# Performance work log

Hardware: AMD Instinct MI355X
Metric: run time of the kernel (lower is better)

Reference implementation:

```python
import jax, jax.numpy as jnp
import numpy as np

D, H, K = 384, 6, 8
B, NQ, NK = 4, 2048, 2048
EPS = 1e-5


def _ln(x, s, b):
    m = jnp.mean(x, axis=-1, keepdims=True)
    v = jnp.mean((x - m) ** 2, axis=-1, keepdims=True)
    return (x - m) * jax.lax.rsqrt(v + EPS) * s + b


def _mha(q, k, v, Wo, bo):
    # q,k,v: [B, N, D]
    dh = D // H
    qh = q.reshape(q.shape[0], q.shape[1], H, dh).transpose(0, 2, 1, 3)
    kh = k.reshape(k.shape[0], k.shape[1], H, dh).transpose(0, 2, 1, 3)
    vh = v.reshape(v.shape[0], v.shape[1], H, dh).transpose(0, 2, 1, 3)
    scores = jnp.einsum('bhqd,bhkd->bhqk', qh, kh) / jnp.sqrt(jnp.asarray(dh, q.dtype))
    attn = jax.nn.softmax(scores, axis=-1)
    out = jnp.einsum('bhqk,bhkd->bhqd', attn, vh)
    out = out.transpose(0, 2, 1, 3).reshape(q.shape[0], q.shape[1], D)
    return out @ Wo + bo


def _knn_edge(q_coords, k_coords, q_feats, k_feats):
    # coords: [B, N, 3]; feats: [B, N, D]. EdgeConv-style feature:
    # concat(neighbor_feat - center_feat, center_feat) -> [B, Nq, K, 2D]
    d2 = (jnp.sum(q_coords ** 2, -1)[:, :, None]
          + jnp.sum(k_coords ** 2, -1)[:, None, :]
          - 2.0 * jnp.einsum('bqc,bkc->bqk', q_coords, k_coords))
    _, idx = jax.lax.top_k(-d2, K)  # [B, Nq, K] nearest neighbors in key set
    neigh = jax.vmap(lambda f, i: f[i])(k_feats, idx)  # [B, Nq, K, D]
    center = jnp.broadcast_to(q_feats[:, :, None, :], neigh.shape)
    return jnp.concatenate([neigh - center, center], axis=-1)


def setup_inputs() -> dict:
    key = jax.random.key(0)
    ks = jax.random.split(key, 24)
    s = 0.02
    return {
        'query_points': jax.random.normal(ks[0], (B, 3 + D, NQ), jnp.float32),
        'key_points': jax.random.normal(ks[1], (B, 3 + D, NK), jnp.float32),
        'ln_in_s': jnp.ones((D,), jnp.float32), 'ln_in_b': jnp.zeros((D,), jnp.float32),
        'qkv_W': jax.random.normal(ks[2], (D, 3 * D), jnp.float32) * s,
        'attn_out_W': jax.random.normal(ks[3], (D, D), jnp.float32) * s,
        'attn_out_b': jnp.zeros((D,), jnp.float32),
        'ff_W1': jax.random.normal(ks[4], (D, 2 * D), jnp.float32) * s,
        'ff_b1': jnp.zeros((2 * D,), jnp.float32),
        'ff_W2': jax.random.normal(ks[5], (2 * D, D), jnp.float32) * s,
        'ff_b2': jnp.zeros((D,), jnp.float32),
        'ffn_s': jnp.ones((D,), jnp.float32), 'ffn_b': jnp.zeros((D,), jnp.float32),
        'knn1_W': jax.random.normal(ks[6], (2 * D, D), jnp.float32) * s,
        'knn1_b': jnp.zeros((D,), jnp.float32),
        'knn2_W': jax.random.normal(ks[7], (2 * D, D), jnp.float32) * s,
        'knn2_b': jnp.zeros((D,), jnp.float32),
        'self_merge_W': jax.random.normal(ks[8], (2 * D, D), jnp.float32) * s,
        'self_merge_b': jnp.zeros((D,), jnp.float32),
        'cross_merge_W': jax.random.normal(ks[9], (2 * D, D), jnp.float32) * s,
        'cross_merge_b': jnp.zeros((D,), jnp.float32),
        'cnq_s': jnp.ones((D,), jnp.float32), 'cnq_b': jnp.zeros((D,), jnp.float32),
        'cnk_s': jnp.ones((D,), jnp.float32), 'cnk_b': jnp.zeros((D,), jnp.float32),
        'cq_W': jax.random.normal(ks[10], (D, D), jnp.float32) * s,
        'ck_W': jax.random.normal(ks[11], (D, D), jnp.float32) * s,
        'cv_W': jax.random.normal(ks[12], (D, D), jnp.float32) * s,
    }


def reference(query_points, key_points, ln_in_s, ln_in_b, qkv_W, attn_out_W,
              attn_out_b, ff_W1, ff_b1, ff_W2, ff_b2, ffn_s, ffn_b,
              knn1_W, knn1_b, knn2_W, knn2_b, self_merge_W, self_merge_b,
              cross_merge_W, cross_merge_b, cnq_s, cnq_b, cnk_s, cnk_b,
              cq_W, ck_W, cv_W):
    qp = jnp.transpose(query_points, (0, 2, 1))  # [B, Nq, 3+D]
    kp = jnp.transpose(key_points, (0, 2, 1))    # [B, Nk, 3+D]
    q_coords, q_feats = qp[..., :3], qp[..., 3:]
    k_coords, k_feats = kp[..., :3], kp[..., 3:]

    # --- self attention + self kNN geometry ---
    norm_f = _ln(q_feats, ln_in_s, ln_in_b)
    qkv = norm_f @ qkv_W
    q, k, v = jnp.split(qkv, 3, axis=-1)
    attn_f = _mha(q, k, v, attn_out_W, attn_out_b)

    edge = _knn_edge(q_coords, q_coords, norm_f, norm_f)          # [B,Nq,K,2D]
    geom = jax.nn.leaky_relu(edge @ knn1_W + knn1_b, 0.2)
    geom = jnp.max(geom, axis=2)                                   # [B,Nq,D]

    attn_f = jnp.concatenate([attn_f, geom], axis=-1) @ self_merge_W + self_merge_b
    q_feats = attn_f + q_feats

    # --- cross attention + cross kNN geometry ---
    nq = _ln(q_feats, cnq_s, cnq_b)
    nk = _ln(k_feats, cnk_s, cnk_b)
    cross_f = _mha(nq @ cq_W, nk @ ck_W, nk @ cv_W, attn_out_W, attn_out_b)

    cedge = _knn_edge(q_coords, k_coords, nq, nk)                  # [B,Nq,K,2D]
    cgeom = jax.nn.leaky_relu(cedge @ knn2_W + knn2_b, 0.2)
    cgeom = jnp.max(cgeom, axis=2)

    cross_f = jnp.concatenate([cross_f, cgeom], axis=-1) @ cross_merge_W + cross_merge_b
    q_feats = q_feats + cross_f

    # --- feed forward ---
    h = _ln(q_feats, ffn_s, ffn_b)
    q_feats = q_feats + (jax.nn.gelu(h @ ff_W1 + ff_b1) @ ff_W2 + ff_b2)

    out = jnp.concatenate([q_coords, q_feats], axis=-1)
    return jnp.transpose(out, (0, 2, 1))  # [B, 3+D, Nq]
```

## Files before the change

### kernel.cpp

```cpp
#include <hip/hip_runtime.h>
#include <cstdint>
#include <cstddef>

#define NB 4
#define NN 2048
#define DD 384
#define NH 6

typedef float f4 __attribute__((ext_vector_type(4)));
typedef float f32x4 __attribute__((ext_vector_type(4)));
typedef short bf16x8 __attribute__((ext_vector_type(8)));
typedef unsigned u32x2 __attribute__((ext_vector_type(2)));

__device__ __forceinline__ float gelu_t(float x) {
  float x3 = x*x*x;
  return 0.5f*x*(1.0f + tanhf(0.7978845608028654f*(x + 0.044715f*x3)));
}

__device__ __forceinline__ unsigned short f2b(float f) {
  unsigned u = __builtin_bit_cast(unsigned, f);
  u += 0x7fffu + ((u >> 16) & 1u);
  return (unsigned short)(u >> 16);
}

__device__ __forceinline__ float b2f(unsigned short u) {
  return __builtin_bit_cast(float, ((unsigned)u) << 16);
}

__device__ __forceinline__ unsigned cvtpk(float a, float b) {
  unsigned r;
  asm("v_cvt_pk_bf16_f32 %0, %1, %2" : "=v"(r) : "v"(a), "v"(b));
  return r;
}

typedef __attribute__((address_space(1))) const void gvoid_t;
typedef __attribute__((address_space(3))) void lvoid_t;
__device__ __forceinline__ void gl16(const void* g, void* l) {
  __builtin_amdgcn_global_load_lds((gvoid_t*)g, (lvoid_t*)l, 16, 0, 0);
}

__device__ __forceinline__ unsigned long long shfl_xor_u64(unsigned long long v, int m) {
  unsigned lo = (unsigned)v, hi = (unsigned)(v >> 32);
  lo = (unsigned)__shfl_xor((int)lo, m);
  hi = (unsigned)__shfl_xor((int)hi, m);
  return ((unsigned long long)hi << 32) | lo;
}

__global__ __launch_bounds__(256) void split_k(const float* __restrict__ pts,
                                               float* __restrict__ coords,
                                               float* __restrict__ feats) {
  __shared__ float t[32][33];
  int b = blockIdx.z;
  int c0 = blockIdx.x*32, n0 = blockIdx.y*32;
  int tx = threadIdx.x, ty = threadIdx.y;
#pragma unroll
  for (int i = 0; i < 4; ++i) {
    int c = c0 + ty + i*8;
    if (c < 387) t[ty+i*8][tx] = pts[((size_t)b*387 + c)*NN + n0 + tx];
  }
  __syncthreads();
#pragma unroll
  for (int i = 0; i < 4; ++i) {
    int n = n0 + ty + i*8;
    int c = c0 + tx;
    if (c < 387) {
      float v = t[tx][ty+i*8];
      if (c < 3) coords[((size_t)b*NN + n)*4 + c] = v;
      else       feats[((size_t)b*NN + n)*DD + (c-3)] = v;
    }
    if (c0 == 0 && tx == 3) {
      float x = t[0][ty+i*8], y = t[1][ty+i*8], z = t[2][ty+i*8];
      coords[((size_t)b*NN + n)*4 + 3] = x*x + y*y + z*z;
    }
  }
}

__global__ __launch_bounds__(256) void pack_k(const float* __restrict__ coords,
                                              const float* __restrict__ feats,
                                              float* __restrict__ out) {
  __shared__ float t[32][33];
  int b = blockIdx.z;
  int c0 = blockIdx.x*32, n0 = blockIdx.y*32;
  int tx = threadIdx.x, ty = threadIdx.y;
#pragma unroll
  for (int i = 0; i < 4; ++i) {
    int n = n0 + ty + i*8;
    int c = c0 + tx;
    if (c < 387) {
      float v = (c < 3) ? coords[((size_t)b*NN + n)*4 + c]
                        : feats[((size_t)b*NN + n)*DD + (c-3)];
      t[tx][ty+i*8] = v;
    }
  }
  __syncthreads();
#pragma unroll
  for (int i = 0; i < 4; ++i) {
    int c = c0 + ty + i*8;
    if (c < 387) out[((size_t)b*387 + c)*NN + n0 + tx] = t[ty+i*8][tx];
  }
}

__device__ __forceinline__ void ln_body(const float* __restrict__ x,
                                        const float* __restrict__ g,
                                        const float* __restrict__ bb,
                                        unsigned short* __restrict__ o,
                                        int row) {
  int lane = threadIdx.x & 63;
  const float* xr = x + (size_t)row*DD;
  float v[6]; float s = 0.f;
#pragma unroll
  for (int i = 0; i < 6; ++i) { v[i] = xr[lane + i*64]; s += v[i]; }
#pragma unroll
  for (int off = 1; off < 64; off <<= 1) s += __shfl_xor(s, off);
  float mean = s * (1.f/384.f);
  float s2 = 0.f;
#pragma unroll
  for (int i = 0; i < 6; ++i) { float d = v[i] - mean; s2 += d*d; }
#pragma unroll
  for (int off = 1; off < 64; off <<= 1) s2 += __shfl_xor(s2, off);
  float rs = rsqrtf(s2*(1.f/384.f) + 1e-5f);
  unsigned short* orow = o + (size_t)row*DD;
#pragma unroll
  for (int i = 0; i < 6; ++i) {
    int c = lane + i*64;
    orow[c] = f2b((v[i]-mean)*rs*g[c] + bb[c]);
  }
}

__global__ __launch_bounds__(256) void ln_k(const float* __restrict__ x,
                                            const float* __restrict__ g,
                                            const float* __restrict__ bb,
                                            unsigned short* __restrict__ o) {
  ln_body(x, g, bb, o, blockIdx.x*4 + (threadIdx.x >> 6));
}

__global__ __launch_bounds__(256) void ln2_k(const float* __restrict__ x1,
                                             const float* __restrict__ g1,
                                             const float* __restrict__ b1,
                                             unsigned short* __restrict__ o1,
                                             const float* __restrict__ x2,
                                             const float* __restrict__ g2,
                                             const float* __restrict__ b2,
                                             unsigned short* __restrict__ o2) {
  int row = blockIdx.x*4 + (threadIdx.x >> 6);
  if (blockIdx.y == 0) ln_body(x1, g1, b1, o1, row);
  else                 ln_body(x2, g2, b2, o2, row);
}

struct WSrcs { const float* p[13]; };

__global__ __launch_bounds__(256) void wtrans_k(WSrcs srcs, unsigned short* __restrict__ dst) {
  constexpr int KK[13]  = {384,384,384,384,768,384,384,384,384,384,768,384,768};
  constexpr int NW[13]  = {1152,384,384,384,384,384,384,384,384,384,384,768,384};
  constexpr int MD[13]  = {0,0,2,0,0,0,0,0,0,2,0,0,0};
  constexpr int OFF[13] = {0,442368,589824,737280,884736,1179648,1327104,1474560,
                           1622016,1769472,1916928,2211840,2506752};
  constexpr int PFX[14] = {0,432,576,720,864,1152,1296,1440,1584,1728,1872,2160,2448,2736};
  int bid = blockIdx.x;
  int e = 0;
  while (bid >= PFX[e+1]) ++e;
  int t = bid - PFX[e];
  int K = KK[e], N = NW[e];
  int ntiles = N >> 5;
  int kt = t / ntiles, nt = t - kt*ntiles;
  const float* src = srcs.p[e];
  __shared__ float T[32][33];
  int tx = threadIdx.x & 31, ty = threadIdx.x >> 5;
  int n = nt*32 + tx;
#pragma unroll
  for (int i = 0; i < 4; ++i) {
    int k = kt*32 + ty + i*8;
    float v = src[(size_t)k*N + n];
    if (MD[e] == 2) v = src[(size_t)(k+384)*N + n] - v;
    T[ty+i*8][tx] = v;
  }
  __syncthreads();
#pragma unroll
  for (int i = 0; i < 4; ++i) {
    int nn = nt*32 + ty + i*8;
    int kk = kt*32 + tx;
    dst[(size_t)OFF[e] + (size_t)nn*K + kk] = f2b(T[tx][ty+i*8]);
  }
}

template<int ACT, int ACC, int OB, int HALFM>
__global__ __launch_bounds__(256) void mgemm_k(const unsigned short* __restrict__ A, int lda,
                                               const unsigned short* __restrict__ Wt,
                                               const float* __restrict__ bias,
                                               void* __restrict__ Cv, int ldc, int cofs,
                                               int Kd) {
  constexpr int BM   = HALFM ? 64 : 128;
  constexpr int MT   = HALFM ? 2 : 4;
  constexpr int AG   = HALFM ? 2 : 4;
  constexpr int ABUF = BM*128;
  constexpr int BUFSZ = ABUF + 8192;
  __shared__ char lds[2*BUFSZ];
  int tid = threadIdx.x;
  int lane = tid & 63, w = tid >> 6, g = lane >> 4, c = lane & 15;
  int wr = w >> 1, wc = w & 1;
  int m0 = blockIdx.y*BM, n0 = blockIdx.x*64;
  int lrow = lane >> 3;
  int cswz = ((lane & 7) ^ lrow)*8;

  f32x4 acc[MT][2];
#pragma unroll
  for (int mt = 0; mt < MT; ++mt)
#pragma unroll
    for (int nt = 0; nt < 2; ++nt) acc[mt][nt] = 0.f;

  int KT = Kd >> 6;
  {
    char* As = lds; char* Bs = lds + ABUF;
#pragma unroll
    for (int i = 0; i < AG; ++i) {
      int rb = i*32 + w*8;
      gl16(A + (size_t)(m0 + rb + lrow)*lda + cswz, As + rb*128);
    }
#pragma unroll
    for (int i = 0; i < 2; ++i) {
      int rb = i*32 + w*8;
      gl16(Wt + (size_t)(n0 + rb + lrow)*Kd + cswz, Bs + rb*128);
    }
  }
  __syncthreads();

  for (int kt = 0; kt < KT; ++kt) {
    char* Asc = lds + (kt & 1)*BUFSZ;
    char* Bsc = Asc + ABUF;
    if (kt + 1 < KT) {
      char* Asn = lds + ((kt + 1) & 1)*BUFSZ;
      char* Bsn = Asn + ABUF;
      int k0 = (kt + 1)*64;
#pragma unroll
      for (int i = 0; i < AG; ++i) {
        int rb = i*32 + w*8;
        gl16(A + (size_t)(m0 + rb + lrow)*lda + k0 + cswz, Asn + rb*128);
      }
#pragma unroll
      for (int i = 0; i < 2; ++i) {
        int rb = i*32 + w*8;
        gl16(Wt + (size_t)(n0 + rb + lrow)*Kd + k0 + cswz, Bsn + rb*128);
      }
    }
#pragma unroll
    for (int kb = 0; kb < 2; ++kb) {
      bf16x8 af[MT], bfr[2];
#pragma unroll
      for (int mt = 0; mt < MT; ++mt) {
        int row = wr*(BM/2) + mt*16 + c;
        int ch = (kb*4 + g) ^ (row & 7);
        af[mt] = *(const bf16x8*)(Asc + row*128 + ch*16);
      }
#pragma unroll
      for (int nt = 0; nt < 2; ++nt) {
        int row = wc*32 + nt*16 + c;
        int ch = (kb*4 + g) ^ (row & 7);
        bfr[nt] = *(const bf16x8*)(Bsc + row*128 + ch*16);
      }
#pragma unroll
      for (int mt = 0; mt < MT; ++mt)
#pragma unroll
        for (int nt = 0; nt < 2; ++nt)
          acc[mt][nt] = __builtin_amdgcn_mfma_f32_16x16x32_bf16(af[mt], bfr[nt], acc[mt][nt], 0, 0, 0);
    }
    __syncthreads();
  }

#pragma unroll
  for (int mt = 0; mt < MT; ++mt) {
#pragma unroll
    for (int nt = 0; nt < 2; ++nt) {
      int coln = n0 + wc*32 + nt*16 + c;
      float bval = bias ? bias[coln] : 0.f;
#pragma unroll
      for (int r = 0; r < 4; ++r) {
        int m = m0 + wr*(BM/2) + mt*16 + 4*g + r;
        float t = acc[mt][nt][r] + bval;
        if (ACT == 1) t = gelu_t(t);
        if (OB) {
          ((unsigned short*)Cv)[(size_t)m*ldc + cofs + coln] = f2b(t);
        } else {
          float* cp = (float*)Cv + (size_t)m*ldc + cofs + coln;
          if (ACC) t += *cp;
          *cp = t;
        }
      }
    }
  }
}

struct FSegs {
  const unsigned short* A[5];
  unsigned short* out[5];
  int ldc[5];
  int cofs[5];
};

__global__ __launch_bounds__(256) void fgemm_k(FSegs fs, const unsigned short* __restrict__ Wt) {
  __shared__ char lds[49152];
  int tid = threadIdx.x;
  int lane = tid & 63, w = tid >> 6, g = lane >> 4, c = lane & 15;
  int wr = w >> 1, wc = w & 1;
  int m0 = blockIdx.y*128, n0 = blockIdx.x*64;
  int seg = n0 / 384;
  const unsigned short* A = fs.A[seg];
  int lrow = lane >> 3;
  int cswz = ((lane & 7) ^ lrow)*8;

  f32x4 acc[4][2];
#pragma unroll
  for (int mt = 0; mt < 4; ++mt)
#pragma unroll
    for (int nt = 0; nt < 2; ++nt) acc[mt][nt] = 0.f;

  {
    char* As = lds; char* Bs = lds + 16384;
#pragma unroll
    for (int i = 0; i < 4; ++i) {
      int rb = i*32 + w*8;
      gl16(A + (size_t)(m0 + rb + lrow)*384 + cswz, As + rb*128);
    }
#pragma unroll
    for (int i = 0; i < 2; ++i) {
      int rb = i*32 + w*8;
      gl16(Wt + (size_t)(n0 + rb + lrow)*384 + cswz, Bs + rb*128);
    }
  }
  __syncthreads();

  for (int kt = 0; kt < 6; ++kt) {
    char* Asc = lds + (kt & 1)*24576;
    char* Bsc = Asc + 16384;
    if (kt + 1 < 6) {
      char* Asn = lds + ((kt + 1) & 1)*24576;
      char* Bsn = Asn + 16384;
      int k0 = (kt + 1)*64;
#pragma unroll
      for (int i = 0; i < 4; ++i) {
        int rb = i*32 + w*8;
        gl16(A + (size_t)(m0 + rb + lrow)*384 + k0 + cswz, Asn + rb*128);
      }
#pragma unroll
      for (int i = 0; i < 2; ++i) {
        int rb = i*32 + w*8;
        gl16(Wt + (size_t)(n0 + rb + lrow)*384 + k0 + cswz, Bsn + rb*128);
      }
    }
#pragma unroll
    for (int kb = 0; kb < 2; ++kb) {
      bf16x8 af[4], bfr[2];
#pragma unroll
      for (int mt = 0; mt < 4; ++mt) {
        int row = wr*64 + mt*16 + c;
        int ch = (kb*4 + g) ^ (row & 7);
        af[mt] = *(const bf16x8*)(Asc + row*128 + ch*16);
      }
#pragma unroll
      for (int nt = 0; nt < 2; ++nt) {
        int row = wc*32 + nt*16 + c;
        int ch = (kb*4 + g) ^ (row & 7);
        bfr[nt] = *(const bf16x8*)(Bsc + row*128 + ch*16);
      }
#pragma unroll
      for (int mt = 0; mt < 4; ++mt)
#pragma unroll
        for (int nt = 0; nt < 2; ++nt)
          acc[mt][nt] = __builtin_amdgcn_mfma_f32_16x16x32_bf16(af[mt], bfr[nt], acc[mt][nt], 0, 0, 0);
    }
    __syncthreads();
  }

  if (seg == 2) {
    unsigned short* vtp = fs.out[2];
    int bb = m0 >> 11;
    int tokb = (m0 & 2047) + wr*64 + 4*g;
#pragma unroll
    for (int mt = 0; mt < 4; ++mt) {
#pragma unroll
      for (int nt = 0; nt < 2; ++nt) {
        int cseg = (n0 - 768) + wc*32 + nt*16 + c;
        int h = cseg >> 6, d = cseg & 63;
        u32x2 pv;
        pv[0] = cvtpk(acc[mt][nt][0], acc[mt][nt][1]);
        pv[1] = cvtpk(acc[mt][nt][2], acc[mt][nt][3]);
        *(u32x2*)(vtp + ((size_t)((bb*NH + h)*64 + d))*NN + tokb + mt*16) = pv;
      }
    }
    return;
  }

  unsigned short* outp = fs.out[seg];
  int ldcs = fs.ldc[seg];
  int cbase = fs.cofs[seg] + (n0 - seg*384);
#pragma unroll
  for (int mt = 0; mt < 4; ++mt) {
#pragma unroll
    for (int nt = 0; nt < 2; ++nt) {
      int coln = cbase + wc*32 + nt*16 + c;
#pragma unroll
      for (int r = 0; r < 4; ++r) {
        int m = m0 + wr*64 + mt*16 + 4*g + r;
        outp[(size_t)m*ldcs + coln] = f2b(acc[mt][nt][r]);
      }
    }
  }
}

__global__ __launch_bounds__(256) void flashm_k(const unsigned short* __restrict__ qkvb,
                                                const unsigned short* __restrict__ vt,
                                                unsigned short* __restrict__ o) {
  __shared__ char smem[40960];
  char* PT = smem + 32768;
  int bid = blockIdx.x;
  int s = (bid & 7)*96 + (bid >> 3);
  int qt = s & 31; int hb = s >> 5;
  int h = hb % NH, b = hb / NH;
  int q0 = qt*64;
  int tid = threadIdx.x;
  int w = tid >> 6, lane = tid & 63, g = lane >> 4, c = lane & 15;
  int lrow = lane >> 3;
  int gsw = ((lane & 7) ^ lrow)*8;

  const unsigned short* kbase = qkvb + (size_t)b*NN*1152 + 384 + h*64;
  const unsigned short* vbase = vt + ((size_t)(b*NH + h))*64*NN;

  bf16x8 qf[2];
  {
    const unsigned short* qrow = qkvb + ((size_t)(b*NN + q0 + w*16 + c))*1152 + h*64;
    qf[0] = *(const bf16x8*)(qrow + 8*g);
    qf[1] = *(const bf16x8*)(qrow + 32 + 8*g);
  }
  f32x4 oacc[4];
#pragma unroll
  for (int i = 0; i < 4; ++i) oacc[i] = 0.f;
  float lsum = 0.f;

#define FSTAGE(bf, ktb) { \
    char* KB = smem + (bf)*16384; char* VB = KB + 8192; \
    gl16(kbase + (size_t)((ktb) + w*16 + lrow)*1152 + gsw,     KB + (w*16)*128); \
    gl16(kbase + (size_t)((ktb) + w*16 + 8 + lrow)*1152 + gsw, KB + (w*16+8)*128); \
    gl16(vbase + (size_t)(w*16 + lrow)*NN + (ktb) + gsw,       VB + (w*16)*128); \
    gl16(vbase + (size_t)(w*16 + 8 + lrow)*NN + (ktb) + gsw,   VB + (w*16+8)*128); }

  FSTAGE(0, 0);
  __syncthreads();

  for (int kt = 0; kt < 32; ++kt) {
    if (kt + 1 < 32) FSTAGE((kt + 1) & 1, (kt + 1)*64);
    char* KTc = smem + (kt & 1)*16384;
    char* VTc = KTc + 8192;

    f32x4 sT[4];
#pragma unroll
    for (int nt = 0; nt < 4; ++nt) sT[nt] = 0.f;
#pragma unroll
    for (int nt = 0; nt < 4; ++nt) {
      int krow = nt*16 + c;
#pragma unroll
      for (int kb = 0; kb < 2; ++kb) {
        int ch = ((kb*4 + g) ^ (krow & 7))*16;
        bf16x8 kf_ = *(const bf16x8*)(KTc + krow*128 + ch);
        sT[nt] = __builtin_amdgcn_mfma_f32_16x16x32_bf16(kf_, qf[kb], sT[nt], 0, 0, 0);
      }
    }

    int prow = w*16 + c;
    int pswz = (c & 7) << 4;
#pragma unroll
    for (int nt = 0; nt < 4; ++nt) {
      float p0 = __builtin_amdgcn_exp2f(sT[nt][0] * 0.18033688011112042f);
      float p1 = __builtin_amdgcn_exp2f(sT[nt][1] * 0.18033688011112042f);
      float p2 = __builtin_amdgcn_exp2f(sT[nt][2] * 0.18033688011112042f);
      float p3 = __builtin_amdgcn_exp2f(sT[nt][3] * 0.18033688011112042f);
      lsum += (p0 + p1) + (p2 + p3);
      u32x2 pk;
      pk[0] = cvtpk(p0, p1);
      pk[1] = cvtpk(p2, p3);
      *(u32x2*)(PT + prow*128 + ((nt*32 + 8*g) ^ pswz)) = pk;
    }

    bf16x8 pb[2];
#pragma unroll
    for (int kb = 0; kb < 2; ++kb)
      pb[kb] = *(const bf16x8*)(PT + prow*128 + (((kb*4 + g) ^ (c & 7))*16));

#pragma unroll
    for (int dt = 0; dt < 4; ++dt) {
      int vrow = dt*16 + c;
#pragma unroll
      for (int kb = 0; kb < 2; ++kb) {
        int ch = ((kb*4 + g) ^ (vrow & 7))*16;
        bf16x8 vf = *(const bf16x8*)(VTc + vrow*128 + ch);
        oacc[dt] = __builtin_amdgcn_mfma_f32_16x16x32_bf16(vf, pb[kb], oacc[dt], 0, 0, 0);
      }
    }
    __syncthreads();
  }
#undef FSTAGE

  lsum += __shfl_xor(lsum, 16);
  lsum += __shfl_xor(lsum, 32);
  float inv = 1.f / lsum;
  size_t orow = ((size_t)b*NN + q0 + w*16 + c)*DD + h*64;
#pragma unroll
  for (int dt = 0; dt < 4; ++dt) {
    u32x2 ov;
    ov[0] = cvtpk(oacc[dt][0]*inv, oacc[dt][1]*inv);
    ov[1] = cvtpk(oacc[dt][2]*inv, oacc[dt][3]*inv);
    *(u32x2*)(o + orow + dt*16 + 4*g) = ov;
  }
}

__global__ __launch_bounds__(256) void knn2_k(const float* __restrict__ qc4,
                                              const float* __restrict__ kc4,
                                              int* __restrict__ idx1,
                                              int* __restrict__ idx2) {
  __shared__ unsigned long long sbuf[4][64];
  const float* kcs = blockIdx.y ? kc4 : qc4;
  int* idxo = blockIdx.y ? idx2 : idx1;
  int lane = threadIdx.x & 63;
  int w = threadIdx.x >> 6;
  int q = blockIdx.x*4 + w;
  int b = q >> 11;
  f4 qv = *(const f4*)(qc4 + (size_t)q*4);
  float mx_ = -2.f*qv[0], my_ = -2.f*qv[1], mz_ = -2.f*qv[2];
  const float* kb = kcs + (size_t)b*NN*4;

  float fv[32];
  float fm = INFINITY;
#pragma unroll
  for (int i = 0; i < 32; ++i) {
    f4 kv = *(const f4*)(kb + (size_t)(lane + i*64)*4);
    float f = fmaf(mx_, kv[0], fmaf(my_, kv[1], fmaf(mz_, kv[2], kv[3])));
    fv[i] = f;
    fm = fminf(fm, f);
  }

  {
    float v = fm;
#pragma unroll
    for (int k = 2; k <= 64; k <<= 1) {
#pragma unroll
      for (int j = k >> 1; j >= 1; j >>= 1) {
        float p = __shfl_xor(v, j);
        bool tmin = (((lane & k) == 0) == ((lane & j) == 0));
        v = tmin ? fminf(v, p) : fmaxf(v, p);
      }
    }
    fm = __shfl(v, 7);
  }
  float T = fm;

  int cnt = 0;
#pragma unroll
  for (int i = 0; i < 32; ++i) {
    bool p = fv[i] <= T;
    unsigned long long mask = __ballot(p);
    if (mask) {
      if (p) {
        int off = cnt + (int)__popcll(mask & ((1ull << lane) - 1ull));
        unsigned u = __builtin_bit_cast(unsigned, fv[i]);
        u ^= 0x80000000u | (unsigned)((int)u >> 31);
        if (off < 64)
          sbuf[w][off] = ((unsigned long long)u << 32) | (unsigned)(lane + i*64);
      }
      cnt += (int)__popcll(mask);
    }
  }

  unsigned long long key = ~0ull;
  if (lane < cnt && lane < 64) key = sbuf[w][lane];
#pragma unroll
  for (int k = 2; k <= 64; k <<= 1) {
#pragma unroll
    for (int j = k >> 1; j >= 1; j >>= 1) {
      unsigned long long p = shfl_xor_u64(key, j);
      bool tmin = (((lane & k) == 0) == ((lane & j) == 0));
      bool less = key < p;
      unsigned long long mn = less ? key : p;
      unsigned long long mx = less ? p : key;
      key = tmin ? mn : mx;
    }
  }
  if (lane < 8) idxo[(size_t)q*8 + lane] = (int)(unsigned)key;
}

__global__ __launch_bounds__(384) void geom_k(const unsigned short* __restrict__ GCb,
                                              const float* __restrict__ bias,
                                              const int* __restrict__ idx,
                                              unsigned short* __restrict__ out) {
  int q = blockIdx.x;
  int b = q >> 11;
  int d = threadIdx.x;
  float c = b2f(GCb[(size_t)q*768 + 384 + d]) + bias[d];
  float mx = -INFINITY;
#pragma unroll
  for (int kn = 0; kn < 8; ++kn) {
    int j = idx[(size_t)q*8 + kn];
    float gg = b2f(GCb[((size_t)(b << 11) + j)*768 + d]);
    float y = gg + c;
    y = (y > 0.f) ? y : 0.2f*y;
    mx = fmaxf(mx, y);
  }
  out[(size_t)q*768 + 384 + d] = f2b(mx);
}

extern "C" void kernel_launch(void* const* d_in, const int* in_sizes, int n_in,
                              void* d_out, int out_size, void* d_ws, size_t ws_size,
                              hipStream_t stream) {
  (void)in_sizes; (void)n_in; (void)out_size; (void)ws_size;
  const float* qpts  = (const float*)d_in[0];
  const float* kpts  = (const float*)d_in[1];
  const float* ln_s  = (const float*)d_in[2];
  const float* ln_b  = (const float*)d_in[3];
  const float* qkvW  = (const float*)d_in[4];
  const float* Wo    = (const float*)d_in[5];
  const float* bo    = (const float*)d_in[6];
  const float* ffW1  = (const float*)d_in[7];
  const float* ffb1  = (const float*)d_in[8];
  const float* ffW2  = (const float*)d_in[9];
  const float* ffb2  = (const float*)d_in[10];
  const float* ffns  = (const float*)d_in[11];
  const float* ffnb  = (const float*)d_in[12];
  const float* knn1W = (const float*)d_in[13];
  const float* knn1b = (const float*)d_in[14];
  const float* knn2W = (const float*)d_in[15];
  const float* knn2b = (const float*)d_in[16];
  const float* smW   = (const float*)d_in[17];
  const float* smb   = (const float*)d_in[18];
  const float* cmW   = (const float*)d_in[19];
  const float* cmb   = (const float*)d_in[20];
  const float* cnqs  = (const float*)d_in[21];
  const float* cnqb  = (const float*)d_in[22];
  const float* cnks  = (const float*)d_in[23];
  const float* cnkb  = (const float*)d_in[24];
  const float* cqW   = (const float*)d_in[25];
  const float* ckW   = (const float*)d_in[26];
  const float* cvW   = (const float*)d_in[27];

  float* ws = (float*)d_ws;
  float* qc4  = ws;
  float* kc4  = qc4 + 32768;
  float* qf   = kc4 + 32768;
  float* kf   = qf + 3145728;
  unsigned short* nrmb = (unsigned short*)(kf + 3145728);
  unsigned short* nkb  = (unsigned short*)(kf + 3145728 + 1572864);
  float* qkv = kf + 3145728 + 1572864 + 1572864;
  unsigned short* qkvb   = (unsigned short*)qkv;
  unsigned short* attnGb = (unsigned short*)qkv;
  unsigned short* vtb    = (unsigned short*)(qkv + 4718592);
  unsigned short* wtb    = (unsigned short*)(qkv + 4718592 + 1572864);
  unsigned short* attnOb = (unsigned short*)(qkv + 4718592 + 1572864 + 1400832);
  unsigned short* GCbb   = (unsigned short*)((float*)attnOb + 1572864);
  int* idx1 = (int*)((float*)GCbb + 3145728);
  int* idx2 = idx1 + 65536;

  const int W_FA=0, W_WO=737280, W_SM=884736, W_FB=1179648,
            W_CM=1916928, W_FF1=2211840, W_FF2=2506752;

  WSrcs srcs;
  srcs.p[0]=qkvW; srcs.p[1]=knn1W; srcs.p[2]=knn1W; srcs.p[3]=Wo; srcs.p[4]=smW;
  srcs.p[5]=cqW; srcs.p[6]=ckW; srcs.p[7]=cvW; srcs.p[8]=knn2W; srcs.p[9]=knn2W;
  srcs.p[10]=cmW; srcs.p[11]=ffW1; srcs.p[12]=ffW2;
  wtrans_k<<<2736, 256, 0, stream>>>(srcs, wtb);

  dim3 tgrid(13, 64, NB), tblk(32, 8);
  split_k<<<tgrid, tblk, 0, stream>>>(qpts, qc4, qf);
  split_k<<<tgrid, tblk, 0, stream>>>(kpts, kc4, kf);

  knn2_k<<<dim3(2048, 2), 256, 0, stream>>>(qc4, kc4, idx1, idx2);

  dim3 mg384h(6, 128), mg768(12, 64), fg(30, 64);

  ln_k<<<2048, 256, 0, stream>>>(qf, ln_s, ln_b, nrmb);
  {
    FSegs fa;
    for (int s = 0; s < 5; ++s) fa.A[s] = nrmb;
    fa.out[0] = qkvb; fa.ldc[0] = 1152; fa.cofs[0] = 0;
    fa.out[1] = qkvb; fa.ldc[1] = 1152; fa.cofs[1] = 384;
    fa.out[2] = vtb;  fa.ldc[2] = 0;    fa.cofs[2] = 0;
    fa.out[3] = GCbb; fa.ldc[3] = 768;  fa.cofs[3] = 0;
    fa.out[4] = GCbb; fa.ldc[4] = 768;  fa.cofs[4] = 384;
    fgemm_k<<<fg, 256, 0, stream>>>(fa, wtb + W_FA);
  }
  flashm_k<<<768, 256, 0, stream>>>(qkvb, vtb, attnOb);
  mgemm_k<0,0,1,1><<<mg384h, 256, 0, stream>>>(attnOb, DD, wtb+W_WO, bo, attnGb, 768, 0, DD);
  geom_k<<<8192, 384, 0, stream>>>(GCbb, knn1b, idx1, attnGb);
  mgemm_k<0,1,0,1><<<mg384h, 256, 0, stream>>>(attnGb, 768, wtb+W_SM, smb, qf, DD, 0, 768);

  ln2_k<<<dim3(2048, 2), 256, 0, stream>>>(qf, cnqs, cnqb, nrmb, kf, cnks, cnkb, nkb);
  {
    FSegs fb;
    fb.A[0] = nrmb; fb.A[1] = nkb; fb.A[2] = nkb; fb.A[3] = nkb; fb.A[4] = nrmb;
    fb.out[0] = qkvb; fb.ldc[0] = 1152; fb.cofs[0] = 0;
    fb.out[1] = qkvb; fb.ldc[1] = 1152; fb.cofs[1] = 384;
    fb.out[2] = vtb;  fb.ldc[2] = 0;    fb.cofs[2] = 0;
    fb.out[3] = GCbb; fb.ldc[3] = 768;  fb.cofs[3] = 0;
    fb.out[4] = GCbb; fb.ldc[4] = 768;  fb.cofs[4] = 384;
    fgemm_k<<<fg, 256, 0, stream>>>(fb, wtb + W_FB);
  }
  flashm_k<<<768, 256, 0, stream>>>(qkvb, vtb, attnOb);
  mgemm_k<0,0,1,1><<<mg384h, 256, 0, stream>>>(attnOb, DD, wtb+W_WO, bo, attnGb, 768, 0, DD);
  geom_k<<<8192, 384, 0, stream>>>(GCbb, knn2b, idx2, attnGb);
  mgemm_k<0,1,0,1><<<mg384h, 256, 0, stream>>>(attnGb, 768, wtb+W_CM, cmb, qf, DD, 0, 768);

  ln_k<<<2048, 256, 0, stream>>>(qf, ffns, ffnb, nrmb);
  mgemm_k<1,0,1,0><<<mg768, 256, 0, stream>>>(nrmb, DD, wtb+W_FF1, ffb1, attnGb, 768, 0, DD);
  mgemm_k<0,1,0,1><<<mg384h, 256, 0, stream>>>(attnGb, 768, wtb+W_FF2, ffb2, qf, DD, 0, 768);

  pack_k<<<tgrid, tblk, 0, stream>>>(qc4, qf, (float*)d_out);
}
```

Before: 317.0 us.

## Restructure flash attention with 32x32 MFMA and split-K across wave pairs

Rewrites the attention kernel so each wave computes a 32-query by 64-key tile with 32x32x16 bf16 MFMAs. The two wave pairs each process alternate key tiles (split-K) with their own double-buffered K/V staging in 80KB of LDS. The partial outputs and row sums are merged through shared memory at the end. It also adds s_setprio around the MFMA blocks. The aim is fewer LDS reads per FLOP and more MFMA density, at the cost of more LDS (lower occupancy) and an extra reduction step.

```diff
diff --git a/kernel.cpp b/kernel.cpp
--- a/kernel.cpp
+++ b/kernel.cpp
@@ -9,6 +9,7 @@
 
 typedef float f4 __attribute__((ext_vector_type(4)));
 typedef float f32x4 __attribute__((ext_vector_type(4)));
+typedef float f32x16 __attribute__((ext_vector_type(16)));
 typedef short bf16x8 __attribute__((ext_vector_type(8)));
 typedef unsigned u32x2 __attribute__((ext_vector_type(2)));
 
@@ -409,105 +410,130 @@
 __global__ __launch_bounds__(256) void flashm_k(const unsigned short* __restrict__ qkvb,
                                                 const unsigned short* __restrict__ vt,
                                                 unsigned short* __restrict__ o) {
-  __shared__ char smem[40960];
-  char* PT = smem + 32768;
+  __shared__ char smem[81920];
   int bid = blockIdx.x;
   int s = (bid & 7)*96 + (bid >> 3);
   int qt = s & 31; int hb = s >> 5;
   int h = hb % NH, b = hb / NH;
   int q0 = qt*64;
   int tid = threadIdx.x;
-  int w = tid >> 6, lane = tid & 63, g = lane >> 4, c = lane & 15;
+  int w = tid >> 6, lane = tid & 63;
+  int p = w >> 1, sub = w & 1;
+  int col = lane & 31, hi = lane >> 5;
   int lrow = lane >> 3;
   int gsw = ((lane & 7) ^ lrow)*8;
+  int csw = (col & 7) << 4;
 
   const unsigned short* kbase = qkvb + (size_t)b*NN*1152 + 384 + h*64;
   const unsigned short* vbase = vt + ((size_t)(b*NH + h))*64*NN;
-
-  bf16x8 qf[2];
+  char* PTw = smem + 65536 + w*4096;
+
+  int qrow = q0 + sub*32 + col;
+  bf16x8 qf[4];
   {
-    const unsigned short* qrow = qkvb + ((size_t)(b*NN + q0 + w*16 + c))*1152 + h*64;
-    qf[0] = *(const bf16x8*)(qrow + 8*g);
-    qf[1] = *(const bf16x8*)(qrow + 32 + 8*g);
-  }
-  f32x4 oacc[4];
-#pragma unroll
-  for (int i = 0; i < 4; ++i) oacc[i] = 0.f;
+    const unsigned short* qr = qkvb + ((size_t)(b*NN + qrow))*1152 + h*64 + 8*hi;
+#pragma unroll
+    for (int kk = 0; kk < 4; ++kk) qf[kk] = *(const bf16x8*)(qr + 16*kk);
+  }
+  f32x16 oacc[2];
+  oacc[0] = 0.f; oacc[1] = 0.f;
   float lsum = 0.f;
 
-#define FSTAGE(bf, ktb) { \
-    char* KB = smem + (bf)*16384; char* VB = KB + 8192; \
-    gl16(kbase + (size_t)((ktb) + w*16 + lrow)*1152 + gsw,     KB + (w*16)*128); \
-    gl16(kbase + (size_t)((ktb) + w*16 + 8 + lrow)*1152 + gsw, KB + (w*16+8)*128); \
-    gl16(vbase + (size_t)(w*16 + lrow)*NN + (ktb) + gsw,       VB + (w*16)*128); \
-    gl16(vbase + (size_t)(w*16 + 8 + lrow)*NN + (ktb) + gsw,   VB + (w*16+8)*128); }
-
-  FSTAGE(0, 0);
+#define FST32(bf, t) { \
+    char* KB_ = smem + p*32768 + (bf)*16384; char* VB_ = KB_ + 8192; \
+    _Pragma("unroll") \
+    for (int i = 0; i < 4; ++i) { \
+      int rb = sub*32 + i*8; \
+      gl16(kbase + (size_t)((t)*64 + rb + lrow)*1152 + gsw, KB_ + rb*128); \
+      gl16(vbase + (size_t)(rb + lrow)*NN + (t)*64 + gsw,   VB_ + rb*128); \
+    } }
+
+  FST32(0, p);
   __syncthreads();
 
-  for (int kt = 0; kt < 32; ++kt) {
-    if (kt + 1 < 32) FSTAGE((kt + 1) & 1, (kt + 1)*64);
-    char* KTc = smem + (kt & 1)*16384;
-    char* VTc = KTc + 8192;
-
-    f32x4 sT[4];
-#pragma unroll
-    for (int nt = 0; nt < 4; ++nt) sT[nt] = 0.f;
-#pragma unroll
-    for (int nt = 0; nt < 4; ++nt) {
-      int krow = nt*16 + c;
-#pragma unroll
-      for (int kb = 0; kb < 2; ++kb) {
-        int ch = ((kb*4 + g) ^ (krow & 7))*16;
-        bf16x8 kf_ = *(const bf16x8*)(KTc + krow*128 + ch);
-        sT[nt] = __builtin_amdgcn_mfma_f32_16x16x32_bf16(kf_, qf[kb], sT[nt], 0, 0, 0);
-      }
-    }
-
-    int prow = w*16 + c;
-    int pswz = (c & 7) << 4;
-#pragma unroll
-    for (int nt = 0; nt < 4; ++nt) {
-      float p0 = __builtin_amdgcn_exp2f(sT[nt][0] * 0.18033688011112042f);
-      float p1 = __builtin_amdgcn_exp2f(sT[nt][1] * 0.18033688011112042f);
-      float p2 = __builtin_amdgcn_exp2f(sT[nt][2] * 0.18033688011112042f);
-      float p3 = __builtin_amdgcn_exp2f(sT[nt][3] * 0.18033688011112042f);
-      lsum += (p0 + p1) + (p2 + p3);
-      u32x2 pk;
-      pk[0] = cvtpk(p0, p1);
-      pk[1] = cvtpk(p2, p3);
-      *(u32x2*)(PT + prow*128 + ((nt*32 + 8*g) ^ pswz)) = pk;
-    }
-
-    bf16x8 pb[2];
-#pragma unroll
-    for (int kb = 0; kb < 2; ++kb)
-      pb[kb] = *(const bf16x8*)(PT + prow*128 + (((kb*4 + g) ^ (c & 7))*16));
-
-#pragma unroll
-    for (int dt = 0; dt < 4; ++dt) {
-      int vrow = dt*16 + c;
-#pragma unroll
-      for (int kb = 0; kb < 2; ++kb) {
-        int ch = ((kb*4 + g) ^ (vrow & 7))*16;
-        bf16x8 vf = *(const bf16x8*)(VTc + vrow*128 + ch);
-        oacc[dt] = __builtin_amdgcn_mfma_f32_16x16x32_bf16(vf, pb[kb], oacc[dt], 0, 0, 0);
-      }
-    }
+  for (int t2 = 0; t2 < 16; ++t2) {
+    if (t2 + 1 < 16) FST32((t2 + 1) & 1, 2*(t2 + 1) + p);
+    char* KB = smem + p*32768 + (t2 & 1)*16384;
+    char* VB = KB + 8192;
+
+    f32x16 sT[2];
+    sT[0] = 0.f; sT[1] = 0.f;
+    __builtin_amdgcn_s_setprio(1);
+#pragma unroll
+    for (int m = 0; m < 2; ++m) {
+#pragma unroll
+      for (int kk = 0; kk < 4; ++kk) {
+        bf16x8 kf_ = *(const bf16x8*)(KB + (32*m + col)*128 + ((32*kk + 16*hi) ^ csw));
+        sT[m] = __builtin_amdgcn_mfma_f32_32x32x16_bf16(kf_, qf[kk], sT[m], 0, 0, 0);
+      }
+    }
+    __builtin_amdgcn_s_setprio(0);
+
+#pragma unroll
+    for (int m = 0; m < 2; ++m) {
+      float pv[16];
+#pragma unroll
+      for (int r = 0; r < 16; ++r) {
+        pv[r] = __builtin_amdgcn_exp2f(sT[m][r] * 0.18033688011112042f);
+        lsum += pv[r];
+      }
+#pragma unroll
+      for (int rq = 0; rq < 4; ++rq) {
+        u32x2 pk;
+        pk[0] = cvtpk(pv[4*rq+0], pv[4*rq+1]);
+        pk[1] = cvtpk(pv[4*rq+2], pv[4*rq+3]);
+        *(u32x2*)(PTw + col*128 + ((64*m + 16*rq + 8*hi) ^ csw)) = pk;
+      }
+    }
+
+    bf16x8 pb[4];
+#pragma unroll
+    for (int kk = 0; kk < 4; ++kk)
+      pb[kk] = *(const bf16x8*)(PTw + col*128 + ((32*kk + 16*hi) ^ csw));
+
+    __builtin_amdgcn_s_setprio(1);
+#pragma unroll
+    for (int m = 0; m < 2; ++m) {
+#pragma unroll
+      for (int kk = 0; kk < 4; ++kk) {
+        bf16x8 vf = *(const bf16x8*)(VB + (32*m + col)*128 + ((32*kk + 16*hi) ^ csw));
+        oacc[m] = __builtin_amdgcn_mfma_f32_32x32x16_bf16(vf, pb[kk], oacc[m], 0, 0, 0);
+      }
+    }
+    __builtin_amdgcn_s_setprio(0);
     __syncthreads();
   }
-#undef FSTAGE
-
-  lsum += __shfl_xor(lsum, 16);
-  lsum += __shfl_xor(lsum, 32);
-  float inv = 1.f / lsum;
-  size_t orow = ((size_t)b*NN + q0 + w*16 + c)*DD + h*64;
-#pragma unroll
-  for (int dt = 0; dt < 4; ++dt) {
-    u32x2 ov;
-    ov[0] = cvtpk(oacc[dt][0]*inv, oacc[dt][1]*inv);
-    ov[1] = cvtpk(oacc[dt][2]*inv, oacc[dt][3]*inv);
-    *(u32x2*)(o + orow + dt*16 + 4*g) = ov;
+#undef FST32
+
+  if (w >= 2) {
+    float* area = (float*)(smem + (w - 2)*16384);
+#pragma unroll
+    for (int m = 0; m < 2; ++m)
+#pragma unroll
+      for (int r = 0; r < 16; ++r) area[(m*16 + r)*64 + lane] = oacc[m][r];
+    area[2048 + lane] = lsum;
+  }
+  __syncthreads();
+  if (w < 2) {
+    float* area = (float*)(smem + w*16384);
+#pragma unroll
+    for (int m = 0; m < 2; ++m)
+#pragma unroll
+      for (int r = 0; r < 16; ++r) oacc[m][r] += area[(m*16 + r)*64 + lane];
+    lsum += area[2048 + lane];
+    lsum += __shfl_xor(lsum, 32);
+    float inv = 1.f / lsum;
+    size_t orow = ((size_t)b*NN + qrow)*DD + h*64;
+#pragma unroll
+    for (int m = 0; m < 2; ++m) {
+#pragma unroll
+      for (int rq = 0; rq < 4; ++rq) {
+        u32x2 ov;
+        ov[0] = cvtpk(oacc[m][4*rq+0]*inv, oacc[m][4*rq+1]*inv);
+        ov[1] = cvtpk(oacc[m][4*rq+2]*inv, oacc[m][4*rq+3]*inv);
+        *(u32x2*)(o + orow + 32*m + 8*rq + 4*hi) = ov;
+      }
+    }
   }
 }
 
```

Measured after the change: 323.3 us. About the same (+2.0%).

## Fuse output projection with kNN geometry kernel and offload softmax row sums to MFMA

Applied to the files above, without the earlier changes.

Merges the attention output-projection GEMM and the geometry max-pool gather into one launch. GEMM tiles and geometry queries are interleaved across the grid so the two independent jobs share the GPU and one launch plus its tail is removed. The softmax scale is folded into the Q columns during the QKV GEMM epilogue, which drops a multiply per score in the flash kernel. The per-row exp sum is computed with an extra MFMA against a ones vector instead of scalar adds and cross-lane shuffles. The risks are extra rounding from scaling Q before bf16 conversion and from summing bf16-rounded probabilities, plus load imbalance in the mixed grid.

```diff
diff --git a/kernel.cpp b/kernel.cpp
--- a/kernel.cpp
+++ b/kernel.cpp
@@ -184,21 +184,20 @@
 }
 
 template<int ACT, int ACC, int OB, int HALFM>
-__global__ __launch_bounds__(256) void mgemm_k(const unsigned short* __restrict__ A, int lda,
-                                               const unsigned short* __restrict__ Wt,
-                                               const float* __restrict__ bias,
-                                               void* __restrict__ Cv, int ldc, int cofs,
-                                               int Kd) {
+__device__ __forceinline__ void mgemm_body(const unsigned short* __restrict__ A, int lda,
+                                           const unsigned short* __restrict__ Wt,
+                                           const float* __restrict__ bias,
+                                           void* __restrict__ Cv, int ldc, int cofs,
+                                           int Kd, int bx, int by, char* lds) {
   constexpr int BM   = HALFM ? 64 : 128;
   constexpr int MT   = HALFM ? 2 : 4;
   constexpr int AG   = HALFM ? 2 : 4;
   constexpr int ABUF = BM*128;
   constexpr int BUFSZ = ABUF + 8192;
-  __shared__ char lds[2*BUFSZ];
   int tid = threadIdx.x;
   int lane = tid & 63, w = tid >> 6, g = lane >> 4, c = lane & 15;
   int wr = w >> 1, wc = w & 1;
-  int m0 = blockIdx.y*BM, n0 = blockIdx.x*64;
+  int m0 = by*BM, n0 = bx*64;
   int lrow = lane >> 3;
   int cswz = ((lane & 7) ^ lrow)*8;
 
@@ -289,6 +288,18 @@
   }
 }
 
+template<int ACT, int ACC, int OB, int HALFM>
+__global__ __launch_bounds__(256) void mgemm_k(const unsigned short* __restrict__ A, int lda,
+                                               const unsigned short* __restrict__ Wt,
+                                               const float* __restrict__ bias,
+                                               void* __restrict__ Cv, int ldc, int cofs,
+                                               int Kd) {
+  constexpr int BM = HALFM ? 64 : 128;
+  __shared__ char lds[2*(BM*128 + 8192)];
+  mgemm_body<ACT,ACC,OB,HALFM>(A, lda, Wt, bias, Cv, ldc, cofs, Kd,
+                               blockIdx.x, blockIdx.y, lds);
+}
+
 struct FSegs {
   const unsigned short* A[5];
   unsigned short* out[5];
@@ -389,6 +400,7 @@
     return;
   }
 
+  float qs = (seg == 0) ? 0.18033688011112042f : 1.0f;
   unsigned short* outp = fs.out[seg];
   int ldcs = fs.ldc[seg];
   int cbase = fs.cofs[seg] + (n0 - seg*384);
@@ -400,7 +412,7 @@
 #pragma unroll
       for (int r = 0; r < 4; ++r) {
         int m = m0 + wr*64 + mt*16 + 4*g + r;
-        outp[(size_t)m*ldcs + coln] = f2b(acc[mt][nt][r]);
+        outp[(size_t)m*ldcs + coln] = f2b(acc[mt][nt][r]*qs);
       }
     }
   }
@@ -430,10 +442,14 @@
     qf[0] = *(const bf16x8*)(qrow + 8*g);
     qf[1] = *(const bf16x8*)(qrow + 32 + 8*g);
   }
+  bf16x8 onesv;
+#pragma unroll
+  for (int i = 0; i < 8; ++i) onesv[i] = (short)0x3F80;
+
   f32x4 oacc[4];
 #pragma unroll
   for (int i = 0; i < 4; ++i) oacc[i] = 0.f;
-  float lsum = 0.f;
+  f32x4 lacc = 0.f;
 
 #define FSTAGE(bf, ktb) { \
     char* KB = smem + (bf)*16384; char* VB = KB + 8192; \
@@ -468,11 +484,10 @@
     int pswz = (c & 7) << 4;
 #pragma unroll
     for (int nt = 0; nt < 4; ++nt) {
-      float p0 = __builtin_amdgcn_exp2f(sT[nt][0] * 0.18033688011112042f);
-      float p1 = __builtin_amdgcn_exp2f(sT[nt][1] * 0.18033688011112042f);
-      float p2 = __builtin_amdgcn_exp2f(sT[nt][2] * 0.18033688011112042f);
-      float p3 = __builtin_amdgcn_exp2f(sT[nt][3] * 0.18033688011112042f);
-      lsum += (p0 + p1) + (p2 + p3);
+      float p0 = __builtin_amdgcn_exp2f(sT[nt][0]);
+      float p1 = __builtin_amdgcn_exp2f(sT[nt][1]);
+      float p2 = __builtin_amdgcn_exp2f(sT[nt][2]);
+      float p3 = __builtin_amdgcn_exp2f(sT[nt][3]);
       u32x2 pk;
       pk[0] = cvtpk(p0, p1);
       pk[1] = cvtpk(p2, p3);
@@ -484,6 +499,9 @@
     for (int kb = 0; kb < 2; ++kb)
       pb[kb] = *(const bf16x8*)(PT + prow*128 + (((kb*4 + g) ^ (c & 7))*16));
 
+    lacc = __builtin_amdgcn_mfma_f32_16x16x32_bf16(onesv, pb[0], lacc, 0, 0, 0);
+    lacc = __builtin_amdgcn_mfma_f32_16x16x32_bf16(onesv, pb[1], lacc, 0, 0, 0);
+
 #pragma unroll
     for (int dt = 0; dt < 4; ++dt) {
       int vrow = dt*16 + c;
@@ -498,9 +516,7 @@
   }
 #undef FSTAGE
 
-  lsum += __shfl_xor(lsum, 16);
-  lsum += __shfl_xor(lsum, 32);
-  float inv = 1.f / lsum;
+  float inv = 1.f / lacc[0];
   size_t orow = ((size_t)b*NN + q0 + w*16 + c)*DD + h*64;
 #pragma unroll
   for (int dt = 0; dt < 4; ++dt) {
@@ -585,24 +601,63 @@
   if (lane < 8) idxo[(size_t)q*8 + lane] = (int)(unsigned)key;
 }
 
-__global__ __launch_bounds__(384) void geom_k(const unsigned short* __restrict__ GCb,
-                                              const float* __restrict__ bias,
-                                              const int* __restrict__ idx,
-                                              unsigned short* __restrict__ out) {
-  int q = blockIdx.x;
+__device__ __forceinline__ void geom_body(const unsigned short* __restrict__ GCb,
+                                          const float* __restrict__ bias,
+                                          const int* __restrict__ idx,
+                                          unsigned short* __restrict__ out,
+                                          int q) {
   int b = q >> 11;
-  int d = threadIdx.x;
-  float c = b2f(GCb[(size_t)q*768 + 384 + d]) + bias[d];
-  float mx = -INFINITY;
-#pragma unroll
-  for (int kn = 0; kn < 8; ++kn) {
-    int j = idx[(size_t)q*8 + kn];
-    float gg = b2f(GCb[((size_t)(b << 11) + j)*768 + d]);
-    float y = gg + c;
-    y = (y > 0.f) ? y : 0.2f*y;
-    mx = fmaxf(mx, y);
-  }
-  out[(size_t)q*768 + 384 + d] = f2b(mx);
+  int t = threadIdx.x;
+  int j[8];
+#pragma unroll
+  for (int k = 0; k < 8; ++k) j[k] = idx[(size_t)q*8 + k];
+  const unsigned short* base = GCb + ((size_t)(b << 11))*768;
+  {
+    float c = b2f(GCb[(size_t)q*768 + 384 + t]) + bias[t];
+    float mx = -INFINITY;
+#pragma unroll
+    for (int k = 0; k < 8; ++k) {
+      float y = b2f(base[(size_t)j[k]*768 + t]) + c;
+      y = (y > 0.f) ? y : 0.2f*y;
+      mx = fmaxf(mx, y);
+    }
+    out[(size_t)q*768 + 384 + t] = f2b(mx);
+  }
+  if (t < 128) {
+    int d = t + 256;
+    float c = b2f(GCb[(size_t)q*768 + 384 + d]) + bias[d];
+    float mx = -INFINITY;
+#pragma unroll
+    for (int k = 0; k < 8; ++k) {
+      float y = b2f(base[(size_t)j[k]*768 + d]) + c;
+      y = (y > 0.f) ? y : 0.2f*y;
+      mx = fmaxf(mx, y);
+    }
+    out[(size_t)q*768 + 384 + d] = f2b(mx);
+  }
+}
+
+__global__ __launch_bounds__(256) void wog_k(const unsigned short* __restrict__ A,
+                                             const unsigned short* __restrict__ Wt,
+                                             const float* __restrict__ wob,
+                                             unsigned short* __restrict__ attnG,
+                                             const unsigned short* __restrict__ GCb,
+                                             const float* __restrict__ gbias,
+                                             const int* __restrict__ idx) {
+  __shared__ char lds[32768];
+  int bid = blockIdx.x;
+  int gq;
+  if (bid < 8448) {
+    int t = bid / 11, r = bid - t*11;
+    if (r == 0) {
+      mgemm_body<0,0,1,1>(A, 384, Wt, wob, attnG, 768, 0, 384, t % 6, t / 6, lds);
+      return;
+    }
+    gq = t*10 + (r - 1);
+  } else {
+    gq = 7680 + (bid - 8448);
+  }
+  geom_body(GCb, gbias, idx, attnG, gq);
 }
 
 extern "C" void kernel_launch(void* const* d_in, const int* in_sizes, int n_in,
@@ -684,8 +739,7 @@
     fgemm_k<<<fg, 256, 0, stream>>>(fa, wtb + W_FA);
   }
   flashm_k<<<768, 256, 0, stream>>>(qkvb, vtb, attnOb);
-  mgemm_k<0,0,1,1><<<mg384h, 256, 0, stream>>>(attnOb, DD, wtb+W_WO, bo, attnGb, 768, 0, DD);
-  geom_k<<<8192, 384, 0, stream>>>(GCbb, knn1b, idx1, attnGb);
+  wog_k<<<8960, 256, 0, stream>>>(attnOb, wtb+W_WO, bo, attnGb, GCbb, knn1b, idx1);
   mgemm_k<0,1,0,1><<<mg384h, 256, 0, stream>>>(attnGb, 768, wtb+W_SM, smb, qf, DD, 0, 768);
 
   ln2_k<<<dim3(2048, 2), 256, 0, stream>>>(qf, cnqs, cnqb, nrmb, kf, cnks, cnkb, nkb);
@@ -700,8 +754,7 @@
     fgemm_k<<<fg, 256, 0, stream>>>(fb, wtb + W_FB);
   }
   flashm_k<<<768, 256, 0, stream>>>(qkvb, vtb, attnOb);
-  mgemm_k<0,0,1,1><<<mg384h, 256, 0, stream>>>(attnOb, DD, wtb+W_WO, bo, attnGb, 768, 0, DD);
-  geom_k<<<8192, 384, 0, stream>>>(GCbb, knn2b, idx2, attnGb);
+  wog_k<<<8960, 256, 0, stream>>>(attnOb, wtb+W_WO, bo, attnGb, GCbb, knn2b, idx2);
   mgemm_k<0,1,0,1><<<mg384h, 256, 0, stream>>>(attnGb, 768, wtb+W_CM, cmb, qf, DD, 0, 768);
 
   ln_k<<<2048, 256, 0, stream>>>(qf, ffns, ffnb, nrmb);
```

Measured after the change: 309.8 us. 2.3% less time.
